# Optimization experiments

Measured on AMD Instinct MI355X. Metric: run time of the kernel, lower is better.

## Reference

```python
import jax, jax.numpy as jnp
import numpy as np
from functools import reduce

H = W = 4096


def setup_inputs() -> dict:
    key = jax.random.key(0)
    prob = jax.random.uniform(key, (1, 1, H, W), dtype=jnp.float32)
    return {"prob": prob}


def _ccl_8conn(binary):
    """Parallel connected-component labeling, 8-connectivity (skimage connectivity=2).

    Labels are (min linear index in component) + 1; background = 0. This is the
    same partition into components as skimage.measure.label, up to a bijective
    relabeling of the positive label ids.
    Algorithm: iterate [3x3 min-propagation + 2x pointer jumping] until fixpoint
    (label-equivalence / union-find style, O(log diameter)-ish sweeps).
    """
    h, w = binary.shape
    BIG = np.int32(h * w + 2)  # sentinel larger than any valid label
    idx = jnp.arange(h * w, dtype=jnp.int32).reshape(h, w) + 1
    lab0 = jnp.where(binary, idx, 0)

    def sweep(lab):
        # min over 3x3 foreground neighborhood (includes self)
        l = jnp.where(binary, lab, BIG)
        p = jnp.pad(l, 1, constant_values=int(BIG))
        neigh = [p[di:di + h, dj:dj + w] for di in range(3) for dj in range(3)]
        m = reduce(jnp.minimum, neigh)
        m = jnp.where(binary, m, 0)
        # pointer jumping: hop to the label of the pixel we currently point at
        flat = m.reshape(-1)
        for _ in range(2):
            flat = jnp.where(flat > 0, flat[jnp.maximum(flat - 1, 0)], 0)
        return flat.reshape(h, w)

    def cond(c):
        return c[1]

    def body(c):
        lab, _ = c
        new = sweep(lab)
        return new, jnp.any(new != lab)

    lab, _ = jax.lax.while_loop(cond, body, (lab0, jnp.array(True)))
    return lab


def reference(prob):
    binary = jnp.squeeze(prob) > 0.5  # (prob > 0.5).float().squeeze()
    return _ccl_8conn(binary)
```

## Files before the change

kernel.cpp:

```cpp
#include <hip/hip_runtime.h>
#include <limits.h>


constexpr int HH = 4096;
constexpr int WW = 4096;
constexpr int NPIX = HH * WW;
constexpr int TILE = 64;
constexpr int BDIM = TILE / 2;
constexpr int NBLK = BDIM * BDIM;

__device__ __forceinline__ int find_root_g(int* P, int x) {
    while (true) {
        int p = P[x];
        if (p == x) return x;
        int gp = P[p];
        if (gp == p) return p;
        atomicMin(&P[x], gp);
        x = gp;
    }
}

__device__ __forceinline__ void unite_g(int* P, int a, int b) {
    while (true) {
        a = find_root_g(P, a);
        b = find_root_g(P, b);
        if (a == b) return;
        if (a > b) { int t = a; a = b; b = t; }
        int old = atomicMin(&P[b], a);
        if (old == b) return;
        b = old;
    }
}

__device__ __forceinline__ int find_root_l(int* L, int x) {
    while (true) {
        int p = L[x];
        if (p == x) return x;
        int gp = L[p];
        if (gp == p) return p;
        atomicMin(&L[x], gp);
        x = gp;
    }
}

__device__ __forceinline__ void unite_l(int* L, int a, int b) {
    while (true) {
        a = find_root_l(L, a);
        b = find_root_l(L, b);
        if (a == b) return;
        if (a > b) { int t = a; a = b; b = t; }
        int old = atomicMin(&L[b], a);
        if (old == b) return;
        b = old;
    }
}

__global__ __launch_bounds__(256) void ccl_local_bke(const float* __restrict__ prob,
                                                     int* __restrict__ P) {
    __shared__ int bmask[NBLK];
    __shared__ int parent[NBLK];
    __shared__ int minpix[NBLK];
    const int tile_c = blockIdx.x * TILE;
    const int tile_r = blockIdx.y * TILE;
    const int tid = threadIdx.x;

    int nib[4];
    #pragma unroll
    for (int k = 0; k < 4; ++k) {
        int b = tid + 256 * k;
        int i = b >> 5, j = b & 31;
        const float* rp = prob + (size_t)(tile_r + 2 * i) * WW + tile_c + 2 * j;
        float2 t = *reinterpret_cast<const float2*>(rp);
        float2 bo = *reinterpret_cast<const float2*>(rp + WW);
        int m = (t.x > 0.5f ? 1 : 0) | (t.y > 0.5f ? 2 : 0) |
                (bo.x > 0.5f ? 4 : 0) | (bo.y > 0.5f ? 8 : 0);
        nib[k] = m;
        bmask[b] = m;
        parent[b] = m ? b : -1;
        minpix[b] = INT_MAX;
    }
    __syncthreads();

    #pragma unroll
    for (int k = 0; k < 4; ++k) {
        int m = nib[k];
        if (!m) continue;
        int b = tid + 256 * k;
        int i = b >> 5, j = b & 31;
        if (j > 0 && (m & 0x5) && (bmask[b - 1] & 0xA)) unite_l(parent, b, b - 1);
        if (i > 0) {
            if ((m & 0x3) && (bmask[b - BDIM] & 0xC)) unite_l(parent, b, b - BDIM);
            if (j > 0        && (m & 0x1) && (bmask[b - BDIM - 1] & 0x8)) unite_l(parent, b, b - BDIM - 1);
            if (j < BDIM - 1 && (m & 0x2) && (bmask[b - BDIM + 1] & 0x4)) unite_l(parent, b, b - BDIM + 1);
        }
    }
    __syncthreads();

    int root[4];
    #pragma unroll
    for (int k = 0; k < 4; ++k) {
        int m = nib[k];
        if (!m) { root[k] = -1; continue; }
        int b = tid + 256 * k;
        int x = b;
        while (true) { int p = parent[x]; if (p == x) break; x = p; }
        root[k] = x;
        int i = b >> 5, j = b & 31;
        int gr = tile_r + 2 * i, gc = tile_c + 2 * j;
        int pm;
        if      (m & 1) pm = gr * WW + gc;
        else if (m & 2) pm = gr * WW + gc + 1;
        else if (m & 4) pm = (gr + 1) * WW + gc;
        else            pm = (gr + 1) * WW + gc + 1;
        atomicMin(&minpix[x], pm);
    }
    __syncthreads();

    #pragma unroll
    for (int k = 0; k < 4; ++k) {
        int b = tid + 256 * k;
        int i = b >> 5, j = b & 31;
        int gr = tile_r + 2 * i, gc = tile_c + 2 * j;
        int m = nib[k];
        int2 top = make_int2(-1, -1), bot = make_int2(-1, -1);
        if (m) {
            int lbl = minpix[root[k]];
            top.x = (m & 1) ? lbl : -1;
            top.y = (m & 2) ? lbl : -1;
            bot.x = (m & 4) ? lbl : -1;
            bot.y = (m & 8) ? lbl : -1;
        }
        *reinterpret_cast<int2*>(P + (size_t)gr * WW + gc) = top;
        *reinterpret_cast<int2*>(P + (size_t)(gr + 1) * WW + gc) = bot;
    }
}

__global__ void ccl_border_h(int* __restrict__ P) {
    int c = blockIdx.x * blockDim.x + threadIdx.x;
    int r = (blockIdx.y + 1) * TILE;
    int i = r * WW + c;
    if (P[i] < 0) return;
    int j = i - WW;
    if (P[j] >= 0) {
        unite_g(P, i, j);
    } else {
        if (c > 0      && P[j - 1] >= 0) unite_g(P, i, j - 1);
        if (c < WW - 1 && P[j + 1] >= 0) unite_g(P, i, j + 1);
    }
}

__global__ void ccl_border_v(int* __restrict__ P) {
    int r = blockIdx.x * blockDim.x + threadIdx.x;
    int c = (blockIdx.y + 1) * TILE;
    int i = r * WW + c;
    if (P[i] < 0) return;
    if (P[i - 1] >= 0) unite_g(P, i, i - 1);
    if (r > 0      && P[i - WW - 1] >= 0) unite_g(P, i, i - WW - 1);
    if (r < HH - 1 && P[i + WW - 1] >= 0) unite_g(P, i, i + WW - 1);
}

__device__ __forceinline__ int resolve_memo(const int* __restrict__ P, int x,
                                            int& ci, int& co) {
    if (x < 0) return 0;
    if (x == ci) return co;
    int r = x;
    while (true) { int p = P[r]; if (p == r) break; r = p; }
    ci = x; co = r + 1;
    return co;
}

__global__ void ccl_final4(const int* __restrict__ P, int* __restrict__ out) {
    int i = (blockIdx.x * blockDim.x + threadIdx.x) * 4;
    int4 v = *reinterpret_cast<const int4*>(P + i);
    int ci = -2, co = 0;
    int4 o;
    o.x = resolve_memo(P, v.x, ci, co);
    o.y = resolve_memo(P, v.y, ci, co);
    o.z = resolve_memo(P, v.z, ci, co);
    o.w = resolve_memo(P, v.w, ci, co);
    *reinterpret_cast<int4*>(out + i) = o;
}

__global__ void ccl_compress(int* __restrict__ P) {
    int i = blockIdx.x * blockDim.x + threadIdx.x;
    int x = P[i];
    if (x < 0) return;
    while (true) { int p = P[x]; if (p == x) break; x = p; }
    P[i] = x;
}

__global__ void ccl_convert(int* __restrict__ P) {
    int i = (blockIdx.x * blockDim.x + threadIdx.x) * 4;
    int4 v = *reinterpret_cast<const int4*>(P + i);
    v.x = (v.x < 0) ? 0 : v.x + 1;
    v.y = (v.y < 0) ? 0 : v.y + 1;
    v.z = (v.z < 0) ? 0 : v.z + 1;
    v.w = (v.w < 0) ? 0 : v.w + 1;
    *reinterpret_cast<int4*>(P + i) = v;
}

extern "C" void kernel_launch(void* const* d_in, const int* in_sizes, int n_in,
                              void* d_out, int out_size, void* d_ws, size_t ws_size,
                              hipStream_t stream) {
    const float* prob = (const float*)d_in[0];
    const bool have_ws = ws_size >= (size_t)NPIX * sizeof(int);
    int* P = have_ws ? (int*)d_ws : (int*)d_out;

    ccl_local_bke<<<dim3(WW / TILE, HH / TILE), dim3(256), 0, stream>>>(prob, P);

    dim3 bb(256);
    ccl_border_h<<<dim3(WW / 256, HH / TILE - 1), bb, 0, stream>>>(P);
    ccl_border_v<<<dim3(HH / 256, WW / TILE - 1), bb, 0, stream>>>(P);

    if (have_ws) {
        ccl_final4<<<dim3(NPIX / 4 / 256), dim3(256), 0, stream>>>(P, (int*)d_out);
    } else {
        ccl_compress<<<dim3(NPIX / 256), dim3(256), 0, stream>>>(P);
        ccl_convert<<<dim3(NPIX / 4 / 256), dim3(256), 0, stream>>>(P);
    }
}
```

Before: 256.0 us.

## Key local union-find by min pixel and merge border kernels into one launch

The local block-CCL now stores tile-relative pixel keys in the parent array, so each root is its component's minimum pixel. This removes the separate root-finding pass, the atomicMin onto minpix, and one barrier. The horizontal and vertical border-merge kernels are combined into a single launch selected by blockIdx.y, saving one launch and letting both sets of unions run concurrently. Concurrent global unions from both directions can add atomic contention, and every local find now pays for key-to-block index conversion.

```diff
diff --git a/kernel.cpp b/kernel.cpp
--- a/kernel.cpp
+++ b/kernel.cpp
@@ -32,34 +32,45 @@
     }
 }
 
-__device__ __forceinline__ int find_root_l(int* L, int x) {
-    while (true) {
-        int p = L[x];
-        if (p == x) return x;
-        int gp = L[p];
+__device__ __forceinline__ int lkey2b(int k) {
+    return ((k >> 7) << 5) | ((k & 63) >> 1);
+}
+
+__device__ __forceinline__ int find_l(int* par, int bk) {
+    while (true) {
+        int xb = lkey2b(bk);
+        int p = par[xb];
+        if (p == bk) return bk;
+        int pb = lkey2b(p);
+        int gp = par[pb];
         if (gp == p) return p;
-        atomicMin(&L[x], gp);
-        x = gp;
-    }
-}
-
-__device__ __forceinline__ void unite_l(int* L, int a, int b) {
-    while (true) {
-        a = find_root_l(L, a);
-        b = find_root_l(L, b);
-        if (a == b) return;
-        if (a > b) { int t = a; a = b; b = t; }
-        int old = atomicMin(&L[b], a);
-        if (old == b) return;
-        b = old;
-    }
+        atomicMin(&par[xb], gp);
+        bk = gp;
+    }
+}
+
+__device__ __forceinline__ void unite_l(int* par, int ka, int kb) {
+    while (true) {
+        ka = find_l(par, ka);
+        kb = find_l(par, kb);
+        if (ka == kb) return;
+        if (ka > kb) { int t = ka; ka = kb; kb = t; }
+        int old = atomicMin(&par[lkey2b(kb)], ka);
+        if (old == kb) return;
+        kb = old;
+    }
+}
+
+__device__ __forceinline__ int bkey(int b, int m) {
+    int base = ((b >> 5) << 7) + ((b & 31) << 1);
+    int off = (m & 1) ? 0 : (m & 2) ? 1 : (m & 4) ? 64 : 65;
+    return base + off;
 }
 
 __global__ __launch_bounds__(256) void ccl_local_bke(const float* __restrict__ prob,
                                                      int* __restrict__ P) {
     __shared__ int bmask[NBLK];
-    __shared__ int parent[NBLK];
-    __shared__ int minpix[NBLK];
+    __shared__ int par[NBLK];
     const int tile_c = blockIdx.x * TILE;
     const int tile_r = blockIdx.y * TILE;
     const int tid = threadIdx.x;
@@ -76,8 +87,7 @@
                 (bo.x > 0.5f ? 4 : 0) | (bo.y > 0.5f ? 8 : 0);
         nib[k] = m;
         bmask[b] = m;
-        parent[b] = m ? b : -1;
-        minpix[b] = INT_MAX;
+        par[b] = m ? bkey(b, m) : -1;
     }
     __syncthreads();
 
@@ -87,32 +97,23 @@
         if (!m) continue;
         int b = tid + 256 * k;
         int i = b >> 5, j = b & 31;
-        if (j > 0 && (m & 0x5) && (bmask[b - 1] & 0xA)) unite_l(parent, b, b - 1);
+        int mk = bkey(b, m);
+        if (j > 0) {
+            int wm = bmask[b - 1];
+            if ((m & 0x5) && (wm & 0xA)) unite_l(par, mk, bkey(b - 1, wm));
+        }
         if (i > 0) {
-            if ((m & 0x3) && (bmask[b - BDIM] & 0xC)) unite_l(parent, b, b - BDIM);
-            if (j > 0        && (m & 0x1) && (bmask[b - BDIM - 1] & 0x8)) unite_l(parent, b, b - BDIM - 1);
-            if (j < BDIM - 1 && (m & 0x2) && (bmask[b - BDIM + 1] & 0x4)) unite_l(parent, b, b - BDIM + 1);
-        }
-    }
-    __syncthreads();
-
-    int root[4];
-    #pragma unroll
-    for (int k = 0; k < 4; ++k) {
-        int m = nib[k];
-        if (!m) { root[k] = -1; continue; }
-        int b = tid + 256 * k;
-        int x = b;
-        while (true) { int p = parent[x]; if (p == x) break; x = p; }
-        root[k] = x;
-        int i = b >> 5, j = b & 31;
-        int gr = tile_r + 2 * i, gc = tile_c + 2 * j;
-        int pm;
-        if      (m & 1) pm = gr * WW + gc;
-        else if (m & 2) pm = gr * WW + gc + 1;
-        else if (m & 4) pm = (gr + 1) * WW + gc;
-        else            pm = (gr + 1) * WW + gc + 1;
-        atomicMin(&minpix[x], pm);
+            int nm = bmask[b - BDIM];
+            if ((m & 0x3) && (nm & 0xC)) unite_l(par, mk, bkey(b - BDIM, nm));
+            if (j > 0) {
+                int nwm = bmask[b - BDIM - 1];
+                if ((m & 0x1) && (nwm & 0x8)) unite_l(par, mk, bkey(b - BDIM - 1, nwm));
+            }
+            if (j < BDIM - 1) {
+                int nem = bmask[b - BDIM + 1];
+                if ((m & 0x2) && (nem & 0x4)) unite_l(par, mk, bkey(b - BDIM + 1, nem));
+            }
+        }
     }
     __syncthreads();
 
@@ -124,39 +125,46 @@
         int m = nib[k];
         int2 top = make_int2(-1, -1), bot = make_int2(-1, -1);
         if (m) {
-            int lbl = minpix[root[k]];
-            top.x = (m & 1) ? lbl : -1;
-            top.y = (m & 2) ? lbl : -1;
-            bot.x = (m & 4) ? lbl : -1;
-            bot.y = (m & 8) ? lbl : -1;
+            int x = bkey(b, m);
+            while (true) {
+                int p = par[lkey2b(x)];
+                if (p == x) break;
+                x = p;
+            }
+            int g = (tile_r + (x >> 6)) * WW + tile_c + (x & 63);
+            top.x = (m & 1) ? g : -1;
+            top.y = (m & 2) ? g : -1;
+            bot.x = (m & 4) ? g : -1;
+            bot.y = (m & 8) ? g : -1;
         }
         *reinterpret_cast<int2*>(P + (size_t)gr * WW + gc) = top;
         *reinterpret_cast<int2*>(P + (size_t)(gr + 1) * WW + gc) = bot;
     }
 }
 
-__global__ void ccl_border_h(int* __restrict__ P) {
-    int c = blockIdx.x * blockDim.x + threadIdx.x;
-    int r = (blockIdx.y + 1) * TILE;
-    int i = r * WW + c;
-    if (P[i] < 0) return;
-    int j = i - WW;
-    if (P[j] >= 0) {
-        unite_g(P, i, j);
+__global__ void ccl_border(int* __restrict__ P) {
+    int idx = blockIdx.x * 256 + threadIdx.x;
+    if (blockIdx.y == 0) {
+        int c = idx & (WW - 1);
+        int r = ((idx >> 12) + 1) * TILE;
+        int i = r * WW + c;
+        if (P[i] < 0) return;
+        int j = i - WW;
+        if (P[j] >= 0) {
+            unite_g(P, i, j);
+        } else {
+            if (c > 0      && P[j - 1] >= 0) unite_g(P, i, j - 1);
+            if (c < WW - 1 && P[j + 1] >= 0) unite_g(P, i, j + 1);
+        }
     } else {
-        if (c > 0      && P[j - 1] >= 0) unite_g(P, i, j - 1);
-        if (c < WW - 1 && P[j + 1] >= 0) unite_g(P, i, j + 1);
-    }
-}
-
-__global__ void ccl_border_v(int* __restrict__ P) {
-    int r = blockIdx.x * blockDim.x + threadIdx.x;
-    int c = (blockIdx.y + 1) * TILE;
-    int i = r * WW + c;
-    if (P[i] < 0) return;
-    if (P[i - 1] >= 0) unite_g(P, i, i - 1);
-    if (r > 0      && P[i - WW - 1] >= 0) unite_g(P, i, i - WW - 1);
-    if (r < HH - 1 && P[i + WW - 1] >= 0) unite_g(P, i, i + WW - 1);
+        int r = idx & (HH - 1);
+        int c = ((idx >> 12) + 1) * TILE;
+        int i = r * WW + c;
+        if (P[i] < 0) return;
+        if (P[i - 1] >= 0) unite_g(P, i, i - 1);
+        if (r > 0      && P[i - WW - 1] >= 0) unite_g(P, i, i - WW - 1);
+        if (r < HH - 1 && P[i + WW - 1] >= 0) unite_g(P, i, i + WW - 1);
+    }
 }
 
 __device__ __forceinline__ int resolve_memo(const int* __restrict__ P, int x,
@@ -208,9 +216,7 @@
 
     ccl_local_bke<<<dim3(WW / TILE, HH / TILE), dim3(256), 0, stream>>>(prob, P);
 
-    dim3 bb(256);
-    ccl_border_h<<<dim3(WW / 256, HH / TILE - 1), bb, 0, stream>>>(P);
-    ccl_border_v<<<dim3(HH / 256, WW / TILE - 1), bb, 0, stream>>>(P);
+    ccl_border<<<dim3((HH / TILE - 1) * WW / 256, 2), dim3(256), 0, stream>>>(P);
 
     if (have_ws) {
         ccl_final4<<<dim3(NPIX / 4 / 256), dim3(256), 0, stream>>>(P, (int*)d_out);
```

Result: slower. 335.6 us (+31.1%).
